# Kernel optimization log

Measured on AMD Instinct MI355X. Metric: run time of the kernel, lower is better.

Reference implementation:

```python
import jax, jax.numpy as jnp
import numpy as np

N_ATOMS = 512
N_MOL = 16
HIDDEN = 128
FILTERS = 128
NUM_RBF = 50
CUTOFF = 10.0
N_LAYERS = 3


def setup_inputs() -> dict:
    key = jax.random.key(0)
    ks = jax.random.split(key, 20)
    s = 0.05
    inp = {
        "atomic_numbers": jax.random.randint(ks[0], (N_ATOMS,), 0, 100),
        "positions": jax.random.uniform(ks[1], (N_ATOMS, 3), jnp.float32) * CUTOFF,
        "batch": jnp.sort(jax.random.randint(ks[2], (N_ATOMS,), 0, N_MOL)),
        # parameters (linear weights stored as [in, out])
        "emb": jax.random.normal(ks[3], (100, HIDDEN), jnp.float32) * s,
        "fw1": jax.random.normal(ks[4], (N_LAYERS, NUM_RBF, FILTERS), jnp.float32) * s,
        "fb1": jnp.zeros((N_LAYERS, FILTERS), jnp.float32),
        "fw2": jax.random.normal(ks[5], (N_LAYERS, FILTERS, FILTERS), jnp.float32) * s,
        "fb2": jnp.zeros((N_LAYERS, FILTERS), jnp.float32),
        "d1w": jax.random.normal(ks[6], (N_LAYERS, HIDDEN, FILTERS), jnp.float32) * s,
        "d1b": jnp.zeros((N_LAYERS, FILTERS), jnp.float32),
        "d2w": jax.random.normal(ks[7], (N_LAYERS, FILTERS, HIDDEN), jnp.float32) * s,
        "d2b": jnp.zeros((N_LAYERS, HIDDEN), jnp.float32),
        "ow1": jax.random.normal(ks[8], (HIDDEN, HIDDEN // 2), jnp.float32) * s,
        "ob1": jnp.zeros((HIDDEN // 2,), jnp.float32),
        "ow2": jax.random.normal(ks[9], (HIDDEN // 2, 1), jnp.float32) * s,
        "ob2": jnp.zeros((1,), jnp.float32),
    }
    return inp


def _schnet_fwd(atomic_numbers, positions, batch, emb, fw1, fb1, fw2, fb2,
                d1w, d1b, d2w, d2b, ow1, ob1, ow2, ob2):
    N = positions.shape[0]
    x = emb[atomic_numbers]                                  # [N, H]

    # all-pairs distances (safe sqrt for the zero diagonal)
    diff = positions[:, None, :] - positions[None, :, :]     # [N, N, 3]
    d2 = jnp.sum(diff * diff, axis=-1)                       # [N, N]
    d = jnp.sqrt(jnp.where(d2 > 0, d2, 1.0))
    d = jnp.where(d2 > 0, d, 0.0)

    eye = jnp.eye(N, dtype=bool)
    valid = (~eye) & (d < CUTOFF)                            # no self-edges, within cutoff

    # gaussian RBF embedding of distances
    centers = jnp.linspace(0.0, CUTOFF, NUM_RBF)             # [R]
    width = CUTOFF / NUM_RBF
    rbf = jnp.exp(-((d[..., None] - centers) ** 2) / (2.0 * width * width))  # [N, N, R]

    # cosine cutoff envelope; zero on invalid edges -> messages identical to edge-list version
    env = 0.5 * (jnp.cos(d * jnp.pi / CUTOFF) + 1.0) * valid.astype(d.dtype)  # [N, N]

    for l in range(N_LAYERS):
        filt = jax.nn.silu(rbf @ fw1[l] + fb1[l]) @ fw2[l] + fb2[l]   # [N, N, F]
        filt = filt * env[..., None]
        xj = x @ d1w[l] + d1b[l]                                      # [N, F] source features
        # message[i,j] = xj[i] * filt[i,j]; scatter-add to destination j
        agg = jnp.einsum('if,ijf->jf', xj, filt)                      # [N, F]
        x = x + agg @ d2w[l] + d2b[l]

    # mean-pool atoms per molecule
    mol_sum = jax.ops.segment_sum(x, batch, num_segments=N_MOL)       # [M, H]
    counts = jax.ops.segment_sum(jnp.ones((N,), x.dtype), batch, num_segments=N_MOL)
    mol = mol_sum / jnp.clip(counts, 1.0)[:, None]

    h = jax.nn.silu(mol @ ow1 + ob1)
    return h @ ow2 + ob2                                              # [M, 1]


def reference(atomic_numbers, positions, batch, emb, fw1, fb1, fw2, fb2,
              d1w, d1b, d2w, d2b, ow1, ob1, ow2, ob2):
    return _schnet_fwd(atomic_numbers, positions, batch, emb, fw1, fb1, fw2, fb2,
                       d1w, d1b, d2w, d2b, ow1, ob1, ow2, ob2)
```

## Files before the change

### kernel.cpp

```cpp
#include <hip/hip_runtime.h>
#include <math.h>

#define N_ATOMS 512
#define N_MOL   16
#define HIDDEN  128
#define FILTERS 128
#define NUM_RBF 50
#define CUTOFF  10.0f
#define N_LAYERS 3

#define KB4    4096
#define NB4    (KB4 + 1)
#define TBPL   65
#define TBLK   (N_LAYERS * TBPL)
#define EMBB   16
#define PI_F   3.14159265358979f
#define DINV   409.6f
#define DSTEP  (CUTOFF / (float)KB4)

__device__ __forceinline__ unsigned short f2bf(float v) {
    unsigned u = __float_as_uint(v);
    u += 0x7fffu + ((u >> 16) & 1u);
    return (unsigned short)(u >> 16);
}

__global__ void __launch_bounds__(256) k_front(
        const int* __restrict__ an, const float* __restrict__ emb,
        const float* __restrict__ d1w, const float* __restrict__ d1b,
        const float* __restrict__ fw1, const float* __restrict__ fb1,
        const float* __restrict__ fw2, const float* __restrict__ fb2,
        float* __restrict__ x, unsigned short* __restrict__ xj,
        unsigned short* __restrict__ tab, float* __restrict__ molsum,
        int* __restrict__ done) {
    __shared__ float          s_rbf[64][NUM_RBF];
    __shared__ unsigned short s_h2[64][FILTERS];
    __shared__ __align__(16) float s_row[32][HIDDEN];
    __shared__ int            s_an[32];
    int bid = blockIdx.x, t = threadIdx.x;

    if (bid == 0) {
        for (int idx = t; idx < N_MOL * HIDDEN; idx += 256) molsum[idx] = 0.f;
        if (t == 0) *done = 0;
    }

    if (bid < TBLK) {
        int l = bid / TBPL, bx = bid - l * TBPL;
        int bin0 = bx * 64;
        const float* w1g = fw1 + (size_t)l * NUM_RBF * FILTERS;
        const float* w2g = fw2 + (size_t)l * FILTERS * FILTERS;
        for (int idx = t; idx < 64 * NUM_RBF; idx += 256) {
            int lb = idx / NUM_RBF, r = idx - lb * NUM_RBF;
            float dd = (bin0 + lb) * DSTEP;
            float cr = r * (CUTOFF / (float)(NUM_RBF - 1));
            float xx = dd - cr;
            s_rbf[lb][r] = __expf(-xx * xx * 12.5f);
        }
        __syncthreads();
        int wv = t >> 6, ln = t & 63;
        int c0 = ln, c1 = ln + 64;
        float h0[16], h1[16];
        float b1v0 = fb1[l * FILTERS + c0], b1v1 = fb1[l * FILTERS + c1];
        #pragma unroll
        for (int bb = 0; bb < 16; bb++) { h0[bb] = b1v0; h1[bb] = b1v1; }
        for (int r = 0; r < NUM_RBF; r++) {
            float w0 = w1g[r * FILTERS + c0];
            float w1v = w1g[r * FILTERS + c1];
            #pragma unroll
            for (int bb = 0; bb < 16; bb++) {
                float rb = s_rbf[wv * 16 + bb][r];
                h0[bb] = fmaf(rb, w0, h0[bb]);
                h1[bb] = fmaf(rb, w1v, h1[bb]);
            }
        }
        #pragma unroll
        for (int bb = 0; bb < 16; bb++) {
            float a0 = h0[bb], a1 = h1[bb];
            s_h2[wv * 16 + bb][c0] = f2bf(a0 / (1.f + __expf(-a0)));
            s_h2[wv * 16 + bb][c1] = f2bf(a1 / (1.f + __expf(-a1)));
        }
        __syncthreads();
        float o0[16], o1[16];
        float b2v0 = fb2[l * FILTERS + c0], b2v1 = fb2[l * FILTERS + c1];
        #pragma unroll
        for (int bb = 0; bb < 16; bb++) { o0[bb] = b2v0; o1[bb] = b2v1; }
        const unsigned int* s_h2u = (const unsigned int*)s_h2;
        for (int hp = 0; hp < 64; hp++) {
            float wa0 = w2g[(2 * hp) * FILTERS + c0];
            float wa1 = w2g[(2 * hp) * FILTERS + c1];
            float wb0 = w2g[(2 * hp + 1) * FILTERS + c0];
            float wb1 = w2g[(2 * hp + 1) * FILTERS + c1];
            #pragma unroll
            for (int bb = 0; bb < 16; bb++) {
                unsigned int hu = s_h2u[(wv * 16 + bb) * 64 + hp];
                float hx = __uint_as_float(hu << 16);
                float hy = __uint_as_float(hu & 0xffff0000u);
                o0[bb] = fmaf(hx, wa0, o0[bb]);  o0[bb] = fmaf(hy, wb0, o0[bb]);
                o1[bb] = fmaf(hx, wa1, o1[bb]);  o1[bb] = fmaf(hy, wb1, o1[bb]);
            }
        }
        size_t base = (size_t)l * NB4 * FILTERS;
        #pragma unroll
        for (int bb = 0; bb < 16; bb++) {
            int bin = bin0 + wv * 16 + bb;
            if (bin <= KB4) {
                float dd = bin * DSTEP;
                float env = (bin >= KB4) ? 0.f : 0.5f * (__cosf(dd * (PI_F / CUTOFF)) + 1.f);
                tab[base + (size_t)bin * FILTERS + c0] = f2bf(o0[bb] * env);
                tab[base + (size_t)bin * FILTERS + c1] = f2bf(o1[bb] * env);
            }
        }
    } else {
        int eb = bid - TBLK;
        int i0 = eb * 32;
        if (t < 32) s_an[t] = an[i0 + t];
        __syncthreads();
        for (int idx = t; idx < 32 * HIDDEN; idx += 256) {
            int a = idx >> 7, c = idx & 127;
            float v = emb[(size_t)s_an[a] * HIDDEN + c];
            s_row[a][c] = v;
            x[(size_t)(i0 + a) * HIDDEN + c] = v;
        }
        __syncthreads();
        int cq = t & 31, ag = t >> 5;
        float o[4][4];
        float4 bv = *(const float4*)(d1b + 4 * cq);
        float bva[4] = { bv.x, bv.y, bv.z, bv.w };
        #pragma unroll
        for (int aa = 0; aa < 4; aa++)
            #pragma unroll
            for (int cc = 0; cc < 4; cc++) o[aa][cc] = bva[cc];
        #pragma unroll 4
        for (int h = 0; h < HIDDEN; h += 2) {
            float4 wA = *(const float4*)(d1w + (size_t)h * FILTERS + 4 * cq);
            float4 wB = *(const float4*)(d1w + (size_t)(h + 1) * FILTERS + 4 * cq);
            float wa[4] = { wA.x, wA.y, wA.z, wA.w };
            float wb[4] = { wB.x, wB.y, wB.z, wB.w };
            #pragma unroll
            for (int aa = 0; aa < 4; aa++) {
                float2 hp = *(const float2*)(&s_row[ag * 4 + aa][h]);
                #pragma unroll
                for (int cc = 0; cc < 4; cc++) {
                    o[aa][cc] = fmaf(hp.x, wa[cc], o[aa][cc]);
                    o[aa][cc] = fmaf(hp.y, wb[cc], o[aa][cc]);
                }
            }
        }
        #pragma unroll
        for (int aa = 0; aa < 4; aa++) {
            int i = i0 + ag * 4 + aa;
            #pragma unroll
            for (int cp = 0; cp < 2; cp++) {
                unsigned int pk = (unsigned)f2bf(o[aa][2 * cp]) |
                                  ((unsigned)f2bf(o[aa][2 * cp + 1]) << 16);
                *(unsigned int*)(xj + (size_t)i * FILTERS + 4 * cq + 2 * cp) = pk;
            }
        }
    }
}

template<int LAST>
__global__ void __launch_bounds__(512) k_layer(const float* __restrict__ pos,
        const unsigned int* __restrict__ tabl, const unsigned int* __restrict__ xj_in,
        float* __restrict__ x, const float* __restrict__ w2, const float* __restrict__ b2,
        const float* __restrict__ w1n, const float* __restrict__ b1n,
        unsigned short* __restrict__ xj_out,
        const int* __restrict__ batch, float* __restrict__ molsum, int* __restrict__ done,
        const float* __restrict__ ow1, const float* __restrict__ ob1,
        const float* __restrict__ ow2, const float* __restrict__ ob2,
        float* __restrict__ out) {
    int bid = blockIdx.x, t = threadIdx.x;
    int j0 = 2 * bid, j1 = j0 + 1;
    int wv = t >> 6, e = t & 63;
    __shared__ unsigned int s_bin[N_ATOMS];
    __shared__ float s_part[2][8][FILTERS];
    __shared__ float s_red[4][FILTERS];
    __shared__ float s_agg[2][FILTERS];
    __shared__ float s_xn[2][HIDDEN];
    __shared__ int   s_cnt;
    {
        float px = pos[3*t], py = pos[3*t+1], pz = pos[3*t+2];
        float ax = pos[3*j0], ay = pos[3*j0+1], az = pos[3*j0+2];
        float bx = pos[3*j1], by = pos[3*j1+1], bz = pos[3*j1+2];
        float d0 = sqrtf((px-ax)*(px-ax) + (py-ay)*(py-ay) + (pz-az)*(pz-az));
        float d1 = sqrtf((px-bx)*(px-bx) + (py-by)*(py-by) + (pz-bz)*(pz-bz));
        unsigned int b0 = (t == j0 || d0 >= CUTOFF) ? KB4 : (unsigned)(int)fmaf(d0, DINV, 0.5f);
        unsigned int b1 = (t == j1 || d1 >= CUTOFF) ? KB4 : (unsigned)(int)fmaf(d1, DINV, 0.5f);
        if (b0 > KB4) b0 = KB4;
        if (b1 > KB4) b1 = KB4;
        s_bin[t] = b0 | (b1 << 16);
    }
    int c = t & 127, seg = t >> 7, jj = seg >> 1, sub = seg & 1;
    float xold = (sub == 0) ? x[(size_t)(jj ? j1 : j0) * HIDDEN + c] : 0.f;
    __syncthreads();
    float a0e = 0.f, a0o = 0.f, a1e = 0.f, a1o = 0.f;
    int i0 = wv * 64;
    for (int ii = 0; ii < 64; ii += 4) {
        #pragma unroll
        for (int r = 0; r < 4; r++) {
            unsigned int pk = s_bin[i0 + ii + r];
            unsigned int bb0 = pk & 0xffffu, bb1 = pk >> 16;
            unsigned int xu = xj_in[(size_t)(i0 + ii + r) * 64 + e];
            unsigned int f0 = tabl[(size_t)bb0 * 64 + e];
            unsigned int f1 = tabl[(size_t)bb1 * 64 + e];
            float xe = __uint_as_float(xu << 16), xo = __uint_as_float(xu & 0xffff0000u);
            float p0e = __uint_as_float(f0 << 16), p0o = __uint_as_float(f0 & 0xffff0000u);
            float p1e = __uint_as_float(f1 << 16), p1o = __uint_as_float(f1 & 0xffff0000u);
            a0e = fmaf(xe, p0e, a0e);  a0o = fmaf(xo, p0o, a0o);
            a1e = fmaf(xe, p1e, a1e);  a1o = fmaf(xo, p1o, a1o);
        }
    }
    s_part[0][wv][2*e] = a0e;  s_part[0][wv][2*e+1] = a0o;
    s_part[1][wv][2*e] = a1e;  s_part[1][wv][2*e+1] = a1o;
    __syncthreads();
    if (t < 256) {
        int pj = t >> 7, cc = t & 127;
        float s = 0.f;
        #pragma unroll
        for (int w8 = 0; w8 < 8; w8++) s += s_part[pj][w8][cc];
        s_agg[pj][cc] = s;
    }
    __syncthreads();
    float v = 0.f;
    #pragma unroll 8
    for (int ff = sub * 64; ff < sub * 64 + 64; ff++)
        v = fmaf(s_agg[jj][ff], w2[(size_t)ff * HIDDEN + c], v);
    s_red[seg][c] = v;
    __syncthreads();
    float xnew = 0.f;
    if (sub == 0) {
        xnew = xold + b2[c] + s_red[jj*2][c] + s_red[jj*2+1][c];
        x[(size_t)(jj ? j1 : j0) * HIDDEN + c] = xnew;
        s_xn[jj][c] = xnew;
    }
    __syncthreads();
    if (!LAST) {
        float a2 = 0.f;
        #pragma unroll 8
        for (int hh = sub * 64; hh < sub * 64 + 64; hh++)
            a2 = fmaf(s_xn[jj][hh], w1n[(size_t)hh * FILTERS + c], a2);
        s_red[seg][c] = a2;
        __syncthreads();
        if (sub == 0)
            xj_out[(size_t)(jj ? j1 : j0) * FILTERS + c] =
                f2bf(b1n[c] + s_red[jj*2][c] + s_red[jj*2+1][c]);
    } else {
        if (sub == 0) atomicAdd(&molsum[(size_t)batch[jj ? j1 : j0] * HIDDEN + c], xnew);
        __syncthreads();
        if (t == 0) atomicAdd(done, 1);
        if (bid < N_MOL) {
            int m = bid;
            if (t == 0) {
                while (atomicAdd(done, 0) < N_ATOMS / 2) __builtin_amdgcn_s_sleep(16);
                s_cnt = 0;
            }
            __syncthreads();
            atomicAdd(&s_cnt, (batch[t] == m) ? 1 : 0);
            __syncthreads();
            int cnt = s_cnt;
            if (t < HIDDEN)
                s_xn[0][t] = atomicAdd(&molsum[(size_t)m * HIDDEN + t], 0.f)
                           / (float)(cnt > 0 ? cnt : 1);
            __syncthreads();
            int o = t & 63, sl = t >> 6;
            float a = 0.f;
            #pragma unroll 8
            for (int h = sl * 16; h < sl * 16 + 16; h++)
                a = fmaf(s_xn[0][h], ow1[h * 64 + o], a);
            float* sr = (float*)s_part;
            sr[sl * 64 + o] = a;
            __syncthreads();
            if (t < 64) {
                float vv = ob1[t];
                #pragma unroll
                for (int s8 = 0; s8 < 8; s8++) vv += sr[s8 * 64 + t];
                float hh = vv / (1.f + __expf(-vv));
                float d2 = hh * ow2[t];
                for (int off = 32; off > 0; off >>= 1) d2 += __shfl_down(d2, off, 64);
                if (t == 0) out[m] = d2 + ob2[0];
            }
        }
    }
}

extern "C" void kernel_launch(void* const* d_in, const int* in_sizes, int n_in,
                              void* d_out, int out_size, void* d_ws, size_t ws_size,
                              hipStream_t stream) {
    const int*   an    = (const int*)  d_in[0];
    const float* pos   = (const float*)d_in[1];
    const int*   batch = (const int*)  d_in[2];
    const float* emb   = (const float*)d_in[3];
    const float* fw1   = (const float*)d_in[4];
    const float* fb1   = (const float*)d_in[5];
    const float* fw2   = (const float*)d_in[6];
    const float* fb2   = (const float*)d_in[7];
    const float* d1w   = (const float*)d_in[8];
    const float* d1b   = (const float*)d_in[9];
    const float* d2w   = (const float*)d_in[10];
    const float* d2b   = (const float*)d_in[11];
    const float* ow1   = (const float*)d_in[12];
    const float* ob1   = (const float*)d_in[13];
    const float* ow2   = (const float*)d_in[14];
    const float* ob2   = (const float*)d_in[15];
    float* out = (float*)d_out;

    float*          x    = (float*)d_ws;
    unsigned short* xjA  = (unsigned short*)(x + N_ATOMS * HIDDEN);
    unsigned short* xjB  = xjA + (size_t)N_ATOMS * FILTERS;
    unsigned short* tab  = xjB + (size_t)N_ATOMS * FILTERS;
    float*          mols = (float*)(tab + (size_t)N_LAYERS * NB4 * FILTERS);
    int*            done = (int*)(mols + N_MOL * HIDDEN);

    k_front<<<TBLK + EMBB, 256, 0, stream>>>(
        an, emb, d1w, d1b, fw1, fb1, fw2, fb2, x, xjA, tab, mols, done);

    const unsigned int* t0 = (const unsigned int*)(tab + (size_t)0 * NB4 * FILTERS);
    const unsigned int* t1 = (const unsigned int*)(tab + (size_t)1 * NB4 * FILTERS);
    const unsigned int* t2 = (const unsigned int*)(tab + (size_t)2 * NB4 * FILTERS);

    k_layer<0><<<N_ATOMS/2, 512, 0, stream>>>(pos, t0, (const unsigned int*)xjA, x,
        d2w + (size_t)0*FILTERS*HIDDEN, d2b + (size_t)0*HIDDEN,
        d1w + (size_t)1*HIDDEN*FILTERS, d1b + (size_t)1*FILTERS, xjB,
        batch, mols, done, ow1, ob1, ow2, ob2, out);
    k_layer<0><<<N_ATOMS/2, 512, 0, stream>>>(pos, t1, (const unsigned int*)xjB, x,
        d2w + (size_t)1*FILTERS*HIDDEN, d2b + (size_t)1*HIDDEN,
        d1w + (size_t)2*HIDDEN*FILTERS, d1b + (size_t)2*FILTERS, xjA,
        batch, mols, done, ow1, ob1, ow2, ob2, out);
    k_layer<1><<<N_ATOMS/2, 512, 0, stream>>>(pos, t2, (const unsigned int*)xjA, x,
        d2w + (size_t)2*FILTERS*HIDDEN, d2b + (size_t)2*HIDDEN,
        d1w, d1b, xjB,
        batch, mols, done, ow1, ob1, ow2, ob2, out);
}
```

Before: 71.58 us.

## Retile filter-table MLP to 32 bins per block with 4x4 register tiles

Halves the number of distance bins per block in the filter-table build (doubling the block count to 129 per layer) and switches the two per-bin MLP matmuls from a 16-bins-by-2-columns register layout to 4 bins by 4 contiguous columns per thread. Weight loads become float4, the hidden activation is kept in fp32 padded shared memory instead of bf16, and table stores are packed as two bf16 values per 32-bit write. This aims to raise parallelism and vectorize memory traffic in the table precompute, at the cost of more blocks re-reading the weight matrices.

```diff
diff --git a/kernel.cpp b/kernel.cpp
--- a/kernel.cpp
+++ b/kernel.cpp
@@ -11,7 +11,7 @@
 
 #define KB4    4096
 #define NB4    (KB4 + 1)
-#define TBPL   65
+#define TBPL   129
 #define TBLK   (N_LAYERS * TBPL)
 #define EMBB   16
 #define PI_F   3.14159265358979f
@@ -32,10 +32,10 @@
         float* __restrict__ x, unsigned short* __restrict__ xj,
         unsigned short* __restrict__ tab, float* __restrict__ molsum,
         int* __restrict__ done) {
-    __shared__ float          s_rbf[64][NUM_RBF];
-    __shared__ unsigned short s_h2[64][FILTERS];
+    __shared__ float s_rbf[32][NUM_RBF];
+    __shared__ __align__(16) float s_H[32][132];
     __shared__ __align__(16) float s_row[32][HIDDEN];
-    __shared__ int            s_an[32];
+    __shared__ int   s_an[32];
     int bid = blockIdx.x, t = threadIdx.x;
 
     if (bid == 0) {
@@ -43,12 +43,14 @@
         if (t == 0) *done = 0;
     }
 
+    int cq = t & 31, ag = t >> 5;
+
     if (bid < TBLK) {
         int l = bid / TBPL, bx = bid - l * TBPL;
-        int bin0 = bx * 64;
+        int bin0 = bx * 32;
         const float* w1g = fw1 + (size_t)l * NUM_RBF * FILTERS;
         const float* w2g = fw2 + (size_t)l * FILTERS * FILTERS;
-        for (int idx = t; idx < 64 * NUM_RBF; idx += 256) {
+        for (int idx = t; idx < 32 * NUM_RBF; idx += 256) {
             int lb = idx / NUM_RBF, r = idx - lb * NUM_RBF;
             float dd = (bin0 + lb) * DSTEP;
             float cr = r * (CUTOFF / (float)(NUM_RBF - 1));
@@ -56,57 +58,73 @@
             s_rbf[lb][r] = __expf(-xx * xx * 12.5f);
         }
         __syncthreads();
-        int wv = t >> 6, ln = t & 63;
-        int c0 = ln, c1 = ln + 64;
-        float h0[16], h1[16];
-        float b1v0 = fb1[l * FILTERS + c0], b1v1 = fb1[l * FILTERS + c1];
-        #pragma unroll
-        for (int bb = 0; bb < 16; bb++) { h0[bb] = b1v0; h1[bb] = b1v1; }
-        for (int r = 0; r < NUM_RBF; r++) {
-            float w0 = w1g[r * FILTERS + c0];
-            float w1v = w1g[r * FILTERS + c1];
-            #pragma unroll
-            for (int bb = 0; bb < 16; bb++) {
-                float rb = s_rbf[wv * 16 + bb][r];
-                h0[bb] = fmaf(rb, w0, h0[bb]);
-                h1[bb] = fmaf(rb, w1v, h1[bb]);
-            }
-        }
-        #pragma unroll
-        for (int bb = 0; bb < 16; bb++) {
-            float a0 = h0[bb], a1 = h1[bb];
-            s_h2[wv * 16 + bb][c0] = f2bf(a0 / (1.f + __expf(-a0)));
-            s_h2[wv * 16 + bb][c1] = f2bf(a1 / (1.f + __expf(-a1)));
-        }
-        __syncthreads();
-        float o0[16], o1[16];
-        float b2v0 = fb2[l * FILTERS + c0], b2v1 = fb2[l * FILTERS + c1];
-        #pragma unroll
-        for (int bb = 0; bb < 16; bb++) { o0[bb] = b2v0; o1[bb] = b2v1; }
-        const unsigned int* s_h2u = (const unsigned int*)s_h2;
-        for (int hp = 0; hp < 64; hp++) {
-            float wa0 = w2g[(2 * hp) * FILTERS + c0];
-            float wa1 = w2g[(2 * hp) * FILTERS + c1];
-            float wb0 = w2g[(2 * hp + 1) * FILTERS + c0];
-            float wb1 = w2g[(2 * hp + 1) * FILTERS + c1];
-            #pragma unroll
-            for (int bb = 0; bb < 16; bb++) {
-                unsigned int hu = s_h2u[(wv * 16 + bb) * 64 + hp];
-                float hx = __uint_as_float(hu << 16);
-                float hy = __uint_as_float(hu & 0xffff0000u);
-                o0[bb] = fmaf(hx, wa0, o0[bb]);  o0[bb] = fmaf(hy, wb0, o0[bb]);
-                o1[bb] = fmaf(hx, wa1, o1[bb]);  o1[bb] = fmaf(hy, wb1, o1[bb]);
+        {
+            float h[4][4];
+            float4 bv = *(const float4*)(fb1 + (size_t)l * FILTERS + 4 * cq);
+            float bva[4] = { bv.x, bv.y, bv.z, bv.w };
+            #pragma unroll
+            for (int aa = 0; aa < 4; aa++)
+                #pragma unroll
+                for (int cc = 0; cc < 4; cc++) h[aa][cc] = bva[cc];
+            #pragma unroll 2
+            for (int r = 0; r < NUM_RBF; r++) {
+                float4 w = *(const float4*)(w1g + (size_t)r * FILTERS + 4 * cq);
+                float wa[4] = { w.x, w.y, w.z, w.w };
+                #pragma unroll
+                for (int aa = 0; aa < 4; aa++) {
+                    float rb = s_rbf[ag * 4 + aa][r];
+                    #pragma unroll
+                    for (int cc = 0; cc < 4; cc++) h[aa][cc] = fmaf(rb, wa[cc], h[aa][cc]);
+                }
+            }
+            __syncthreads();
+            #pragma unroll
+            for (int aa = 0; aa < 4; aa++) {
+                float4 sv;
+                sv.x = h[aa][0] / (1.f + __expf(-h[aa][0]));
+                sv.y = h[aa][1] / (1.f + __expf(-h[aa][1]));
+                sv.z = h[aa][2] / (1.f + __expf(-h[aa][2]));
+                sv.w = h[aa][3] / (1.f + __expf(-h[aa][3]));
+                *(float4*)(&s_H[ag * 4 + aa][4 * cq]) = sv;
+            }
+        }
+        __syncthreads();
+        float o[4][4];
+        float4 b2v = *(const float4*)(fb2 + (size_t)l * FILTERS + 4 * cq);
+        float b2a[4] = { b2v.x, b2v.y, b2v.z, b2v.w };
+        #pragma unroll
+        for (int aa = 0; aa < 4; aa++)
+            #pragma unroll
+            for (int cc = 0; cc < 4; cc++) o[aa][cc] = b2a[cc];
+        #pragma unroll 4
+        for (int hh = 0; hh < FILTERS; hh += 2) {
+            float4 wA = *(const float4*)(w2g + (size_t)hh * FILTERS + 4 * cq);
+            float4 wB = *(const float4*)(w2g + (size_t)(hh + 1) * FILTERS + 4 * cq);
+            float wa[4] = { wA.x, wA.y, wA.z, wA.w };
+            float wb[4] = { wB.x, wB.y, wB.z, wB.w };
+            #pragma unroll
+            for (int aa = 0; aa < 4; aa++) {
+                float2 hp = *(const float2*)(&s_H[ag * 4 + aa][hh]);
+                #pragma unroll
+                for (int cc = 0; cc < 4; cc++) {
+                    o[aa][cc] = fmaf(hp.x, wa[cc], o[aa][cc]);
+                    o[aa][cc] = fmaf(hp.y, wb[cc], o[aa][cc]);
+                }
             }
         }
         size_t base = (size_t)l * NB4 * FILTERS;
         #pragma unroll
-        for (int bb = 0; bb < 16; bb++) {
-            int bin = bin0 + wv * 16 + bb;
+        for (int aa = 0; aa < 4; aa++) {
+            int bin = bin0 + ag * 4 + aa;
             if (bin <= KB4) {
                 float dd = bin * DSTEP;
                 float env = (bin >= KB4) ? 0.f : 0.5f * (__cosf(dd * (PI_F / CUTOFF)) + 1.f);
-                tab[base + (size_t)bin * FILTERS + c0] = f2bf(o0[bb] * env);
-                tab[base + (size_t)bin * FILTERS + c1] = f2bf(o1[bb] * env);
+                #pragma unroll
+                for (int cp = 0; cp < 2; cp++) {
+                    unsigned int pk = (unsigned)f2bf(o[aa][2 * cp] * env) |
+                                      ((unsigned)f2bf(o[aa][2 * cp + 1] * env) << 16);
+                    *(unsigned int*)(tab + base + (size_t)bin * FILTERS + 4 * cq + 2 * cp) = pk;
+                }
             }
         }
     } else {
@@ -121,7 +139,6 @@
             x[(size_t)(i0 + a) * HIDDEN + c] = v;
         }
         __syncthreads();
-        int cq = t & 31, ag = t >> 5;
         float o[4][4];
         float4 bv = *(const float4*)(d1b + 4 * cq);
         float bva[4] = { bv.x, bv.y, bv.z, bv.w };
```

After: 63.93 us. -10.7%, faster.
